# Kernel optimization log

Measured on AMD Instinct MI355X. Metric: run time of the kernel, lower is better.

## Reference

```python
import jax, jax.numpy as jnp
import numpy as np
from jax import lax

WIN = 9
PAD = WIN // 2


def _box_sum(x):
    # x: [B,1,H,W]; all-ones WINxWIN conv, stride 1, pad PAD -> same spatial size
    k = jnp.ones((1, 1, WIN, WIN), dtype=x.dtype)
    return lax.conv_general_dilated(
        x, k, window_strides=(1, 1), padding=[(PAD, PAD), (PAD, PAD)],
        dimension_numbers=("NCHW", "OIHW", "NCHW"))


def setup_inputs() -> dict:
    key = jax.random.key(0)
    k1, k2 = jax.random.split(key)
    B, C, H, W = 32, 1, 512, 512
    y_true = jax.random.uniform(k1, (B, C, H, W), dtype=jnp.float32)
    y_pred = jax.random.uniform(k2, (B, C, H, W), dtype=jnp.float32)
    return {"y_true": y_true, "y_pred": y_pred}


def reference(y_true, y_pred):
    Ii, Ji = y_true, y_pred
    win_size = float(WIN * WIN)
    I_sum = _box_sum(Ii)
    J_sum = _box_sum(Ji)
    I2_sum = _box_sum(Ii * Ii)
    J2_sum = _box_sum(Ji * Ji)
    IJ_sum = _box_sum(Ii * Ji)
    u_I = I_sum / win_size
    u_J = J_sum / win_size
    cross = IJ_sum - u_J * I_sum - u_I * J_sum + u_I * u_J * win_size
    I_var = I2_sum - 2.0 * u_I * I_sum + u_I * u_I * win_size
    J_var = J2_sum - 2.0 * u_J * J_sum + u_J * u_J * win_size
    cc = cross * cross / (I_var * J_var + 1e-05)
    return -jnp.mean(cc)
```

## Files before the change

### kernel.cpp

```cpp
#include <hip/hip_runtime.h>


#define BATCH   32
#define IMH     512
#define IMW     512
#define SH      28
#define NSTRIP  19
#define NROWS   36
#define NPART   (BATCH * NSTRIP)

__global__ __launch_bounds__(256) void ncc_main(const float* __restrict__ I,
                                                const float* __restrict__ J,
                                                float* __restrict__ partial) {
    const int t  = threadIdx.x;
    const int s  = blockIdx.x;
    const int b  = blockIdx.y;
    const int r0 = s * SH;
    const float inv81 = 1.0f / 81.0f;

    const float* Ib = I + (size_t)b * IMH * IMW;
    const float* Jb = J + (size_t)b * IMH * IMW;

    const int cbase = 2 * t - 4;

    float2 ring[9][5];
#pragma unroll
    for (int j = 0; j < 9; ++j)
#pragma unroll
        for (int q = 0; q < 5; ++q) ring[j][q] = make_float2(0.f, 0.f);

    float2 V[5];
#pragma unroll
    for (int q = 0; q < 5; ++q) V[q] = make_float2(0.f, 0.f);

    float2 acc = make_float2(0.f, 0.f);

#pragma unroll 1
    for (int g = 0; g < 4; ++g) {
#pragma unroll
        for (int j = 0; j < 9; ++j) {
            const int i  = g * 9 + j;
            const int ri = r0 - 4 + i;

            float vI[10], vJ[10];
            if ((unsigned)ri < (unsigned)IMH) {
                const float* rowI = Ib + (size_t)ri * IMW;
                const float* rowJ = Jb + (size_t)ri * IMW;
#pragma unroll
                for (int k = 0; k < 5; ++k) {
                    const int ck = cbase + 2 * k;
                    if ((unsigned)ck < (unsigned)IMW) {
                        float2 iv = *(const float2*)(rowI + ck);
                        float2 jv = *(const float2*)(rowJ + ck);
                        vI[2 * k] = iv.x; vI[2 * k + 1] = iv.y;
                        vJ[2 * k] = jv.x; vJ[2 * k + 1] = jv.y;
                    } else {
                        vI[2 * k] = 0.f; vI[2 * k + 1] = 0.f;
                        vJ[2 * k] = 0.f; vJ[2 * k + 1] = 0.f;
                    }
                }
            } else {
#pragma unroll
                for (int m = 0; m < 10; ++m) { vI[m] = 0.f; vJ[m] = 0.f; }
            }

            float sI = 0.f, sJ = 0.f, sII = 0.f, sJJ = 0.f, sIJ = 0.f;
#pragma unroll
            for (int m = 0; m < 9; ++m) {
                sI  += vI[m];
                sJ  += vJ[m];
                sII += vI[m] * vI[m];
                sJJ += vJ[m] * vJ[m];
                sIJ += vI[m] * vJ[m];
            }
            const float i0 = vI[0], j0 = vJ[0], i9 = vI[9], j9 = vJ[9];
            float2 Hn[5];
            Hn[0] = make_float2(sI,  sI  + i9      - i0);
            Hn[1] = make_float2(sJ,  sJ  + j9      - j0);
            Hn[2] = make_float2(sII, sII + i9 * i9 - i0 * i0);
            Hn[3] = make_float2(sJJ, sJJ + j9 * j9 - j0 * j0);
            Hn[4] = make_float2(sIJ, sIJ + i9 * j9 - i0 * j0);

#pragma unroll
            for (int q = 0; q < 5; ++q) {
                const float2 old = ring[j][q];
                ring[j][q] = Hn[q];
                V[q].x += Hn[q].x - old.x;
                V[q].y += Hn[q].y - old.y;
            }

            if (i >= 8) {
                const int r = r0 + i - 8;
                if (r < IMH) {
                    {
                        const float aI = V[0].x, aJ = V[1].x;
                        const float cross = V[4].x - aI * aJ * inv81;
                        const float iv    = V[2].x - aI * aI * inv81;
                        const float jv    = V[3].x - aJ * aJ * inv81;
                        acc.x += cross * cross *
                                 __builtin_amdgcn_rcpf(iv * jv + 1e-5f);
                    }
                    {
                        const float aI = V[0].y, aJ = V[1].y;
                        const float cross = V[4].y - aI * aJ * inv81;
                        const float iv    = V[2].y - aI * aI * inv81;
                        const float jv    = V[3].y - aJ * aJ * inv81;
                        acc.y += cross * cross *
                                 __builtin_amdgcn_rcpf(iv * jv + 1e-5f);
                    }
                }
            }
        }
    }

    float sum = acc.x + acc.y;
#pragma unroll
    for (int off = 32; off > 0; off >>= 1) sum += __shfl_down(sum, off, 64);

    __shared__ float wsum[4];
    if ((t & 63) == 0) wsum[t >> 6] = sum;
    __syncthreads();
    if (t == 0) {
        partial[(size_t)b * NSTRIP + s] = wsum[0] + wsum[1] + wsum[2] + wsum[3];
    }
}

__global__ __launch_bounds__(256) void ncc_reduce(const float* __restrict__ partial,
                                                  float* __restrict__ out) {
    const int t = threadIdx.x;
    double ssum = 0.0;
    for (int idx = t; idx < NPART; idx += 256) ssum += (double)partial[idx];
#pragma unroll
    for (int off = 32; off > 0; off >>= 1) ssum += __shfl_down(ssum, off, 64);

    __shared__ double wsum[4];
    if ((t & 63) == 0) wsum[t >> 6] = ssum;
    __syncthreads();
    if (t == 0) {
        const double total = wsum[0] + wsum[1] + wsum[2] + wsum[3];
        out[0] = (float)(-total / 8388608.0);
    }
}

extern "C" void kernel_launch(void* const* d_in, const int* in_sizes, int n_in,
                              void* d_out, int out_size, void* d_ws, size_t ws_size,
                              hipStream_t stream) {
    const float* I = (const float*)d_in[0];
    const float* J = (const float*)d_in[1];
    float* partial = (float*)d_ws;
    float* out     = (float*)d_out;

    dim3 grid(NSTRIP, BATCH);
    ncc_main<<<grid, 256, 0, stream>>>(I, J, partial);
    ncc_reduce<<<1, 256, 0, stream>>>(partial, out);
}
```

Measured before the change: 124.6 us.

## Use shorter row strips and fuse final reduction via atomic last-block pattern

Cuts the strip height from 28 to 10 rows, so the grid grows from 19 to 52 strips per image and fills more of the GPU, at the cost of recomputing more halo rows per strip. The separate reduction kernel is removed. Each block now atomically adds its partial sum to a global accumulator, and the last block to finish writes the output. This adds a memset launch, and float atomics make the sum order nondeterministic and single precision instead of double.

```diff
diff --git a/kernel.cpp b/kernel.cpp
--- a/kernel.cpp
+++ b/kernel.cpp
@@ -4,14 +4,16 @@
 #define BATCH   32
 #define IMH     512
 #define IMW     512
-#define SH      28
-#define NSTRIP  19
-#define NROWS   36
-#define NPART   (BATCH * NSTRIP)
+#define SH      10
+#define NSTRIP  52
+#define NROWS   18
+#define NBLOCKS (BATCH * NSTRIP)
 
 __global__ __launch_bounds__(256) void ncc_main(const float* __restrict__ I,
                                                 const float* __restrict__ J,
-                                                float* __restrict__ partial) {
+                                                float* __restrict__ acc_ws,
+                                                unsigned* __restrict__ cnt_ws,
+                                                float* __restrict__ out) {
     const int t  = threadIdx.x;
     const int s  = blockIdx.x;
     const int b  = blockIdx.y;
@@ -36,7 +38,7 @@
     float2 acc = make_float2(0.f, 0.f);
 
 #pragma unroll 1
-    for (int g = 0; g < 4; ++g) {
+    for (int g = 0; g < 2; ++g) {
 #pragma unroll
         for (int j = 0; j < 9; ++j) {
             const int i  = g * 9 + j;
@@ -121,24 +123,14 @@
     if ((t & 63) == 0) wsum[t >> 6] = sum;
     __syncthreads();
     if (t == 0) {
-        partial[(size_t)b * NSTRIP + s] = wsum[0] + wsum[1] + wsum[2] + wsum[3];
-    }
-}
-
-__global__ __launch_bounds__(256) void ncc_reduce(const float* __restrict__ partial,
-                                                  float* __restrict__ out) {
-    const int t = threadIdx.x;
-    double ssum = 0.0;
-    for (int idx = t; idx < NPART; idx += 256) ssum += (double)partial[idx];
-#pragma unroll
-    for (int off = 32; off > 0; off >>= 1) ssum += __shfl_down(ssum, off, 64);
-
-    __shared__ double wsum[4];
-    if ((t & 63) == 0) wsum[t >> 6] = ssum;
-    __syncthreads();
-    if (t == 0) {
-        const double total = wsum[0] + wsum[1] + wsum[2] + wsum[3];
-        out[0] = (float)(-total / 8388608.0);
+        const float bsum = wsum[0] + wsum[1] + wsum[2] + wsum[3];
+        atomicAdd(acc_ws, bsum);
+        __threadfence();
+        const unsigned old = atomicAdd(cnt_ws, 1u);
+        if (old == (unsigned)(NBLOCKS - 1)) {
+            const float total = atomicAdd(acc_ws, 0.0f);
+            out[0] = -total / 8388608.0f;
+        }
     }
 }
 
@@ -147,10 +139,12 @@
                               hipStream_t stream) {
     const float* I = (const float*)d_in[0];
     const float* J = (const float*)d_in[1];
-    float* partial = (float*)d_ws;
+    float* acc_ws  = (float*)d_ws;
+    unsigned* cnt  = (unsigned*)d_ws + 1;
     float* out     = (float*)d_out;
 
+    hipMemsetAsync(d_ws, 0, 2 * sizeof(float), stream);
+
     dim3 grid(NSTRIP, BATCH);
-    ncc_main<<<grid, 256, 0, stream>>>(I, J, partial);
-    ncc_reduce<<<1, 256, 0, stream>>>(partial, out);
+    ncc_main<<<grid, 256, 0, stream>>>(I, J, acc_ws, cnt, out);
 }
```

After: 175.5 us. 1.41x slower.
